# Optimization experiments

Hardware: AMD Instinct MI355X
Metric: run time of the kernel (lower is better)

The kernel has to match this reference:

```python
import jax, jax.numpy as jnp
import numpy as np

N_NODES, N_EDGES, N_GRAPHS = 20000, 640000, 16
D_NODE = D_EDGE = D_GLOBAL = 64
IN_DIM, LATENT, OUT_DIM = 256, 128, 64


def setup_inputs() -> dict:
    key = jax.random.key(0)
    ks = jax.random.split(key, 12)
    node_attr = jax.random.normal(ks[0], (N_NODES, D_NODE), dtype=jnp.float32)
    edge_attr = jax.random.normal(ks[1], (N_EDGES, D_EDGE), dtype=jnp.float32)
    global_attr = jax.random.normal(ks[2], (N_GRAPHS, D_GLOBAL), dtype=jnp.float32)
    node_mask = jax.random.uniform(ks[3], (N_NODES,), dtype=jnp.float32)
    edge_mask = jax.random.uniform(ks[4], (N_EDGES,), dtype=jnp.float32)
    edge_index = jax.random.randint(ks[5], (2, N_EDGES), 0, N_NODES, dtype=jnp.int64)
    eg_index = jax.random.randint(ks[6], (N_EDGES,), 0, N_GRAPHS, dtype=jnp.int64)
    # MLP params: Linear(IN_DIM, LATENT) -> ReLU -> Linear(LATENT, OUT_DIM)
    s1 = 1.0 / np.sqrt(IN_DIM)
    s2 = 1.0 / np.sqrt(LATENT)
    W1 = jax.random.uniform(ks[7], (IN_DIM, LATENT), minval=-s1, maxval=s1, dtype=jnp.float32)
    b1 = jax.random.uniform(ks[8], (LATENT,), minval=-s1, maxval=s1, dtype=jnp.float32)
    W2 = jax.random.uniform(ks[9], (LATENT, OUT_DIM), minval=-s2, maxval=s2, dtype=jnp.float32)
    b2 = jax.random.uniform(ks[10], (OUT_DIM,), minval=-s2, maxval=s2, dtype=jnp.float32)
    return {"node_attr": node_attr, "edge_attr": edge_attr, "global_attr": global_attr,
            "node_mask": node_mask, "edge_mask": edge_mask,
            "edge_index": edge_index, "eg_index": eg_index,
            "W1": W1, "b1": b1, "W2": W2, "b2": b2}


def reference(node_attr, edge_attr, global_attr, node_mask, edge_mask,
              edge_index, eg_index, W1, b1, W2, b2):
    senders, receivers = edge_index[0], edge_index[1]
    masked_nodes = node_attr * node_mask[:, None]          # [N, d_n]
    senders_attr = masked_nodes[senders]                   # [E, d_n] gather
    receivers_attr = masked_nodes[receivers]               # [E, d_n] gather
    globals_exp = global_attr[eg_index]                    # [E, d_g] gather
    collected = jnp.concatenate(
        [edge_attr, senders_attr, receivers_attr, globals_exp], axis=-1)  # [E, IN_DIM]
    h = jax.nn.relu(collected @ W1 + b1)                   # [E, LATENT]
    out = h @ W2 + b2                                      # [E, OUT_DIM]
    return edge_mask[:, None] * out
```

## Files before the change

kernel.cpp:

```cpp
#include <hip/hip_runtime.h>
#include <stdint.h>

typedef __attribute__((ext_vector_type(8))) short short8;
typedef __attribute__((ext_vector_type(4))) float floatx4;
typedef unsigned short ushort_t;

#define E_TOTAL 640000
#define M_BLK   128
#define XS_LD   264
#define HS_LD   136

__device__ __forceinline__ unsigned short f2h(float f){
    _Float16 h = (_Float16)f;
    union { _Float16 h; unsigned short u; } v; v.h = h; return v.u;
}
__device__ __forceinline__ unsigned pk2h(float a, float b){
    return (unsigned)f2h(a) | ((unsigned)f2h(b) << 16);
}

__global__ void repack_w(const float* __restrict__ W1,
                         const float* __restrict__ W2,
                         ushort_t* __restrict__ W1p,
                         ushort_t* __restrict__ W2p){
    int tid = blockIdx.x * 256 + threadIdx.x;
    if (tid < 8*8*64){
        int kt = tid >> 9, nt = (tid >> 6) & 7, l = tid & 63;
        int q = l >> 4, c = l & 15;
        ushort_t tmp[8];
        #pragma unroll
        for (int j = 0; j < 8; j++)
            tmp[j] = f2h(W1[(kt*32 + q*8 + j)*128 + nt*16 + c]);
        #pragma unroll
        for (int j = 0; j < 8; j++) W1p[tid*8 + j] = tmp[j];
    } else if (tid < 8*8*64 + 4*4*64){
        int t = tid - 8*8*64;
        int kt = t >> 8, nt = (t >> 6) & 3, l = t & 63;
        int q = l >> 4, c = l & 15;
        ushort_t tmp[8];
        #pragma unroll
        for (int j = 0; j < 8; j++)
            tmp[j] = f2h(W2[(kt*32 + q*8 + j)*64 + nt*16 + c]);
        #pragma unroll
        for (int j = 0; j < 8; j++) W2p[t*8 + j] = tmp[j];
    }
}

__global__ __launch_bounds__(512, 4)
void edge_mlp(const float* __restrict__ node_attr,
              const float* __restrict__ edge_attr,
              const float* __restrict__ global_attr,
              const float* __restrict__ node_mask,
              const float* __restrict__ edge_mask,
              const int*   __restrict__ edge_index,
              const int*   __restrict__ eg_index,
              const float* __restrict__ b1,
              const float* __restrict__ b2,
              const ushort_t* __restrict__ W1p,
              const ushort_t* __restrict__ W2p,
              float*       __restrict__ out){
    __shared__ ushort_t Xs[M_BLK * XS_LD];
    ushort_t* Hs = Xs;

    const int tid = threadIdx.x;
    const int e0  = blockIdx.x * M_BLK;

    {
        const float4* src = (const float4*)(edge_attr + (size_t)e0 * 64);
        #pragma unroll
        for (int k = 0; k < 4; k++){
            int idx = tid + k*512;
            int r = idx >> 4, c = idx & 15;
            float4 v = src[idx];
            uint2 o; o.x = pk2h(v.x, v.y); o.y = pk2h(v.z, v.w);
            *(uint2*)&Xs[r*XS_LD + c*4] = o;
        }
    }
    {
        #pragma unroll
        for (int k = 0; k < 4; k++){
            int idx = tid + k*512; int r = idx >> 4, c = idx & 15;
            int g = eg_index[e0 + r];
            const float4* src = (const float4*)(global_attr + (size_t)g * 64);
            float4 v = src[c];
            uint2 o; o.x = pk2h(v.x, v.y); o.y = pk2h(v.z, v.w);
            *(uint2*)&Xs[r*XS_LD + 192 + c*4] = o;
        }
    }
    {
        int r = tid >> 2, seg = (tid >> 1) & 1, half = tid & 1;
        int idx = edge_index[seg*E_TOTAL + e0 + r];
        float m = node_mask[idx];
        const float4* src = (const float4*)(node_attr + (size_t)idx * 64) + half*8;
        ushort_t* dst = &Xs[r*XS_LD + 64 + seg*64 + half*32];
        #pragma unroll
        for (int c2 = 0; c2 < 8; c2++){
            float4 v = src[c2];
            uint2 o; o.x = pk2h(v.x*m, v.y*m); o.y = pk2h(v.z*m, v.w*m);
            *(uint2*)(dst + c2*4) = o;
        }
    }
    __syncthreads();

    const int w  = tid >> 6, lane = tid & 63;
    const int q  = lane >> 4, cc = lane & 15;
    const int mt0 = (w >> 2) * 4;
    const int nt0 = (w & 3) * 2;

    floatx4 acc[4][2];
    #pragma unroll
    for (int i = 0; i < 4; i++)
        #pragma unroll
        for (int j = 0; j < 2; j++) acc[i][j] = (floatx4){0.f,0.f,0.f,0.f};

    const short8* W1v = (const short8*)W1p;
    #pragma unroll
    for (int kt = 0; kt < 8; kt++){
        short8 b[2];
        #pragma unroll
        for (int j = 0; j < 2; j++) b[j] = W1v[(kt*8 + nt0 + j)*64 + lane];
        #pragma unroll
        for (int i = 0; i < 4; i++){
            const short8 a = *(const short8*)&Xs[((mt0 + i)*16 + cc)*XS_LD + kt*32 + q*8];
            #pragma unroll
            for (int j = 0; j < 2; j++)
                acc[i][j] = __builtin_amdgcn_mfma_f32_16x16x32_f16(a, b[j], acc[i][j], 0, 0, 0);
        }
    }
    __syncthreads();

    #pragma unroll
    for (int j = 0; j < 2; j++){
        int col = (nt0 + j)*16 + cc;
        float bb = b1[col];
        #pragma unroll
        for (int i = 0; i < 4; i++){
            int rowb = (mt0 + i)*16 + q*4;
            #pragma unroll
            for (int r = 0; r < 4; r++){
                float v = acc[i][j][r] + bb;
                v = v > 0.f ? v : 0.f;
                Hs[(rowb + r)*HS_LD + col] = f2h(v);
            }
        }
    }
    __syncthreads();

    const int mt20 = (w >> 1) * 2;
    const int nt20 = (w & 1) * 2;

    floatx4 acc2[2][2];
    #pragma unroll
    for (int i = 0; i < 2; i++)
        #pragma unroll
        for (int j = 0; j < 2; j++) acc2[i][j] = (floatx4){0.f,0.f,0.f,0.f};

    const short8* W2v = (const short8*)W2p;
    #pragma unroll
    for (int kt = 0; kt < 4; kt++){
        short8 b[2];
        #pragma unroll
        for (int j = 0; j < 2; j++) b[j] = W2v[(kt*4 + nt20 + j)*64 + lane];
        #pragma unroll
        for (int i = 0; i < 2; i++){
            const short8 a = *(const short8*)&Hs[((mt20 + i)*16 + cc)*HS_LD + kt*32 + q*8];
            #pragma unroll
            for (int j = 0; j < 2; j++)
                acc2[i][j] = __builtin_amdgcn_mfma_f32_16x16x32_f16(a, b[j], acc2[i][j], 0, 0, 0);
        }
    }

    float bb2[2];
    #pragma unroll
    for (int j = 0; j < 2; j++) bb2[j] = b2[(nt20 + j)*16 + cc];
    #pragma unroll
    for (int i = 0; i < 2; i++){
        #pragma unroll
        for (int r = 0; r < 4; r++){
            int row = (mt20 + i)*16 + q*4 + r;
            float em = edge_mask[e0 + row];
            size_t base = (size_t)(e0 + row) * 64;
            #pragma unroll
            for (int j = 0; j < 2; j++){
                float v = (acc2[i][j][r] + bb2[j]) * em;
                out[base + (nt20 + j)*16 + cc] = v;
            }
        }
    }
}

extern "C" void kernel_launch(void* const* d_in, const int* in_sizes, int n_in,
                              void* d_out, int out_size, void* d_ws, size_t ws_size,
                              hipStream_t stream){
    const float* node_attr   = (const float*)d_in[0];
    const float* edge_attr   = (const float*)d_in[1];
    const float* global_attr = (const float*)d_in[2];
    const float* node_mask   = (const float*)d_in[3];
    const float* edge_mask   = (const float*)d_in[4];
    const int*   edge_index  = (const int*)d_in[5];
    const int*   eg_index    = (const int*)d_in[6];
    const float* W1          = (const float*)d_in[7];
    const float* b1          = (const float*)d_in[8];
    const float* W2          = (const float*)d_in[9];
    const float* b2          = (const float*)d_in[10];

    ushort_t* W1p = (ushort_t*)d_ws;
    ushort_t* W2p = W1p + 8*8*64*8;

    repack_w<<<20, 256, 0, stream>>>(W1, W2, W1p, W2p);
    edge_mlp<<<E_TOTAL / M_BLK, 512, 0, stream>>>(
        node_attr, edge_attr, global_attr, node_mask, edge_mask,
        edge_index, eg_index, b1, b2, W1p, W2p, (float*)d_out);
}
```

Baseline: 381.6 us.

## Make edge MLP kernel persistent with register-prefetched gathers for next tile

Switches from one block per 128-edge tile to a persistent grid of 512 blocks that loop over tiles. While the MFMA stages of the current tile run, the node, edge and global rows for the next tile are loaded into registers, and the indices are fetched two tiles ahead. This aims to hide global gather latency behind compute and to amortize bias loads and block launch cost. In exchange it raises register pressure with launch_bounds(512,4), which may cause spills or lower occupancy, and it relies on only 512 blocks to keep the device busy.

```diff
diff --git a/kernel.cpp b/kernel.cpp
--- a/kernel.cpp
+++ b/kernel.cpp
@@ -7,6 +7,8 @@
 
 #define E_TOTAL 640000
 #define M_BLK   128
+#define N_TILES (E_TOTAL / M_BLK)
+#define GRID_P  512
 #define XS_LD   264
 #define HS_LD   136
 
@@ -61,130 +63,203 @@
     __shared__ ushort_t Xs[M_BLK * XS_LD];
     ushort_t* Hs = Xs;
 
-    const int tid = threadIdx.x;
-    const int e0  = blockIdx.x * M_BLK;
+    const int tid  = threadIdx.x;
+    const int w    = tid >> 6, lane = tid & 63;
+    const int q    = lane >> 4, cc = lane & 15;
+    const int mt0  = (w >> 2) * 4;
+    const int nt0  = (w & 3) * 2;
+    const int mt20 = (w >> 1) * 2;
+    const int nt20 = (w & 1) * 2;
+
+    const int nr = tid >> 2, nseg = (tid >> 1) & 1, nhalf = tid & 1;
+
+    float bb1v[2], bb2v[2];
+    #pragma unroll
+    for (int j = 0; j < 2; j++){
+        bb1v[j] = b1[(nt0  + j)*16 + cc];
+        bb2v[j] = b2[(nt20 + j)*16 + cc];
+    }
+
+    const short8* W1v = (const short8*)W1p;
+    const short8* W2v = (const short8*)W2p;
+
+    int t = blockIdx.x;
+
+    uint2 pn16[8];
+    uint2 pe16[4];
+    uint2 pg16[4];
+    int   ei_n;
+    int   eg_n[4];
 
     {
-        const float4* src = (const float4*)(edge_attr + (size_t)e0 * 64);
+        size_t e0 = (size_t)t * M_BLK;
+        int ei = edge_index[nseg*E_TOTAL + e0 + nr];
+        int eg[4];
+        #pragma unroll
+        for (int k = 0; k < 4; k++) eg[k] = eg_index[e0 + ((tid + k*512) >> 4)];
+        float nm = node_mask[ei];
+        const floatx4* nsrc = (const floatx4*)(node_attr + (size_t)ei*64) + nhalf*8;
+        floatx4 nraw[8], eraw[4], graw[4];
+        #pragma unroll
+        for (int c2 = 0; c2 < 8; c2++) nraw[c2] = nsrc[c2];
+        const floatx4* esrc = (const floatx4*)(edge_attr + e0*64);
+        #pragma unroll
+        for (int k = 0; k < 4; k++) eraw[k] = esrc[tid + k*512];
+        #pragma unroll
+        for (int k = 0; k < 4; k++)
+            graw[k] = ((const floatx4*)(global_attr + (size_t)eg[k]*64))[(tid + k*512) & 15];
+        #pragma unroll
+        for (int c2 = 0; c2 < 8; c2++){
+            pn16[c2].x = pk2h(nraw[c2].x*nm, nraw[c2].y*nm);
+            pn16[c2].y = pk2h(nraw[c2].z*nm, nraw[c2].w*nm);
+        }
         #pragma unroll
         for (int k = 0; k < 4; k++){
-            int idx = tid + k*512;
-            int r = idx >> 4, c = idx & 15;
-            float4 v = src[idx];
-            uint2 o; o.x = pk2h(v.x, v.y); o.y = pk2h(v.z, v.w);
-            *(uint2*)&Xs[r*XS_LD + c*4] = o;
-        }
-    }
-    {
+            pe16[k].x = pk2h(eraw[k].x, eraw[k].y); pe16[k].y = pk2h(eraw[k].z, eraw[k].w);
+            pg16[k].x = pk2h(graw[k].x, graw[k].y); pg16[k].y = pk2h(graw[k].z, graw[k].w);
+        }
+    }
+    ei_n = 0; eg_n[0] = eg_n[1] = eg_n[2] = eg_n[3] = 0;
+    if (t + GRID_P < N_TILES){
+        size_t e0n = (size_t)(t + GRID_P) * M_BLK;
+        ei_n = edge_index[nseg*E_TOTAL + e0n + nr];
+        #pragma unroll
+        for (int k = 0; k < 4; k++) eg_n[k] = eg_index[e0n + ((tid + k*512) >> 4)];
+    }
+
+    for (; t < N_TILES; t += GRID_P){
+        const size_t e0 = (size_t)t * M_BLK;
+        const bool hn  = (t +   GRID_P < N_TILES);
+        const bool hn2 = (t + 2*GRID_P < N_TILES);
+
+        __syncthreads();
+
+        {
+            ushort_t* dst = &Xs[nr*XS_LD + 64 + nseg*64 + nhalf*32];
+            #pragma unroll
+            for (int c2 = 0; c2 < 8; c2++) *(uint2*)(dst + c2*4) = pn16[c2];
+        }
         #pragma unroll
         for (int k = 0; k < 4; k++){
             int idx = tid + k*512; int r = idx >> 4, c = idx & 15;
-            int g = eg_index[e0 + r];
-            const float4* src = (const float4*)(global_attr + (size_t)g * 64);
-            float4 v = src[c];
-            uint2 o; o.x = pk2h(v.x, v.y); o.y = pk2h(v.z, v.w);
-            *(uint2*)&Xs[r*XS_LD + 192 + c*4] = o;
-        }
-    }
-    {
-        int r = tid >> 2, seg = (tid >> 1) & 1, half = tid & 1;
-        int idx = edge_index[seg*E_TOTAL + e0 + r];
-        float m = node_mask[idx];
-        const float4* src = (const float4*)(node_attr + (size_t)idx * 64) + half*8;
-        ushort_t* dst = &Xs[r*XS_LD + 64 + seg*64 + half*32];
-        #pragma unroll
-        for (int c2 = 0; c2 < 8; c2++){
-            float4 v = src[c2];
-            uint2 o; o.x = pk2h(v.x*m, v.y*m); o.y = pk2h(v.z*m, v.w*m);
-            *(uint2*)(dst + c2*4) = o;
-        }
-    }
-    __syncthreads();
-
-    const int w  = tid >> 6, lane = tid & 63;
-    const int q  = lane >> 4, cc = lane & 15;
-    const int mt0 = (w >> 2) * 4;
-    const int nt0 = (w & 3) * 2;
-
-    floatx4 acc[4][2];
-    #pragma unroll
-    for (int i = 0; i < 4; i++)
-        #pragma unroll
-        for (int j = 0; j < 2; j++) acc[i][j] = (floatx4){0.f,0.f,0.f,0.f};
-
-    const short8* W1v = (const short8*)W1p;
-    #pragma unroll
-    for (int kt = 0; kt < 8; kt++){
-        short8 b[2];
-        #pragma unroll
-        for (int j = 0; j < 2; j++) b[j] = W1v[(kt*8 + nt0 + j)*64 + lane];
-        #pragma unroll
-        for (int i = 0; i < 4; i++){
-            const short8 a = *(const short8*)&Xs[((mt0 + i)*16 + cc)*XS_LD + kt*32 + q*8];
-            #pragma unroll
-            for (int j = 0; j < 2; j++)
-                acc[i][j] = __builtin_amdgcn_mfma_f32_16x16x32_f16(a, b[j], acc[i][j], 0, 0, 0);
-        }
-    }
-    __syncthreads();
-
-    #pragma unroll
-    for (int j = 0; j < 2; j++){
-        int col = (nt0 + j)*16 + cc;
-        float bb = b1[col];
-        #pragma unroll
-        for (int i = 0; i < 4; i++){
-            int rowb = (mt0 + i)*16 + q*4;
+            *(uint2*)&Xs[r*XS_LD + c*4]       = pe16[k];
+            *(uint2*)&Xs[r*XS_LD + 192 + c*4] = pg16[k];
+        }
+        __syncthreads();
+
+        float nm_n = 0.f;
+        floatx4 nraw[8];
+        if (hn){
+            nm_n = node_mask[ei_n];
+            const floatx4* nsrc = (const floatx4*)(node_attr + (size_t)ei_n*64) + nhalf*8;
+            #pragma unroll
+            for (int c2 = 0; c2 < 8; c2++) nraw[c2] = nsrc[c2];
+        }
+        int ei_n2 = 0, eg_n2[4] = {0,0,0,0};
+        if (hn2){
+            size_t e0n2 = (size_t)(t + 2*GRID_P) * M_BLK;
+            ei_n2 = edge_index[nseg*E_TOTAL + e0n2 + nr];
+            #pragma unroll
+            for (int k = 0; k < 4; k++) eg_n2[k] = eg_index[e0n2 + ((tid + k*512) >> 4)];
+        }
+
+        floatx4 acc[4][2];
+        #pragma unroll
+        for (int i = 0; i < 4; i++)
+            #pragma unroll
+            for (int j = 0; j < 2; j++) acc[i][j] = (floatx4){0.f,0.f,0.f,0.f};
+
+        #pragma unroll
+        for (int kt = 0; kt < 8; kt++){
+            short8 b[2];
+            #pragma unroll
+            for (int j = 0; j < 2; j++) b[j] = W1v[(kt*8 + nt0 + j)*64 + lane];
+            #pragma unroll
+            for (int i = 0; i < 4; i++){
+                const short8 a = *(const short8*)&Xs[((mt0 + i)*16 + cc)*XS_LD + kt*32 + q*8];
+                #pragma unroll
+                for (int j = 0; j < 2; j++)
+                    acc[i][j] = __builtin_amdgcn_mfma_f32_16x16x32_f16(a, b[j], acc[i][j], 0, 0, 0);
+            }
+        }
+
+        floatx4 eraw[4], graw[4];
+        if (hn){
+            #pragma unroll
+            for (int c2 = 0; c2 < 8; c2++){
+                pn16[c2].x = pk2h(nraw[c2].x*nm_n, nraw[c2].y*nm_n);
+                pn16[c2].y = pk2h(nraw[c2].z*nm_n, nraw[c2].w*nm_n);
+            }
+            size_t e0n = (size_t)(t + GRID_P) * M_BLK;
+            const floatx4* esrc = (const floatx4*)(edge_attr + e0n*64);
+            #pragma unroll
+            for (int k = 0; k < 4; k++) eraw[k] = esrc[tid + k*512];
+            #pragma unroll
+            for (int k = 0; k < 4; k++)
+                graw[k] = ((const floatx4*)(global_attr + (size_t)eg_n[k]*64))[(tid + k*512) & 15];
+        }
+
+        __syncthreads();
+
+        #pragma unroll
+        for (int j = 0; j < 2; j++){
+            int col = (nt0 + j)*16 + cc;
+            #pragma unroll
+            for (int i = 0; i < 4; i++){
+                int rowb = (mt0 + i)*16 + q*4;
+                #pragma unroll
+                for (int r = 0; r < 4; r++){
+                    float v = acc[i][j][r] + bb1v[j];
+                    v = v > 0.f ? v : 0.f;
+                    Hs[(rowb + r)*HS_LD + col] = f2h(v);
+                }
+            }
+        }
+        __syncthreads();
+
+        floatx4 acc2[2][2];
+        #pragma unroll
+        for (int i = 0; i < 2; i++)
+            #pragma unroll
+            for (int j = 0; j < 2; j++) acc2[i][j] = (floatx4){0.f,0.f,0.f,0.f};
+
+        #pragma unroll
+        for (int kt = 0; kt < 4; kt++){
+            short8 b[2];
+            #pragma unroll
+            for (int j = 0; j < 2; j++) b[j] = W2v[(kt*4 + nt20 + j)*64 + lane];
+            #pragma unroll
+            for (int i = 0; i < 2; i++){
+                const short8 a = *(const short8*)&Hs[((mt20 + i)*16 + cc)*HS_LD + kt*32 + q*8];
+                #pragma unroll
+                for (int j = 0; j < 2; j++)
+                    acc2[i][j] = __builtin_amdgcn_mfma_f32_16x16x32_f16(a, b[j], acc2[i][j], 0, 0, 0);
+            }
+        }
+
+        #pragma unroll
+        for (int i = 0; i < 2; i++){
             #pragma unroll
             for (int r = 0; r < 4; r++){
-                float v = acc[i][j][r] + bb;
-                v = v > 0.f ? v : 0.f;
-                Hs[(rowb + r)*HS_LD + col] = f2h(v);
-            }
-        }
-    }
-    __syncthreads();
-
-    const int mt20 = (w >> 1) * 2;
-    const int nt20 = (w & 1) * 2;
-
-    floatx4 acc2[2][2];
-    #pragma unroll
-    for (int i = 0; i < 2; i++)
-        #pragma unroll
-        for (int j = 0; j < 2; j++) acc2[i][j] = (floatx4){0.f,0.f,0.f,0.f};
-
-    const short8* W2v = (const short8*)W2p;
-    #pragma unroll
-    for (int kt = 0; kt < 4; kt++){
-        short8 b[2];
-        #pragma unroll
-        for (int j = 0; j < 2; j++) b[j] = W2v[(kt*4 + nt20 + j)*64 + lane];
-        #pragma unroll
-        for (int i = 0; i < 2; i++){
-            const short8 a = *(const short8*)&Hs[((mt20 + i)*16 + cc)*HS_LD + kt*32 + q*8];
-            #pragma unroll
-            for (int j = 0; j < 2; j++)
-                acc2[i][j] = __builtin_amdgcn_mfma_f32_16x16x32_f16(a, b[j], acc2[i][j], 0, 0, 0);
-        }
-    }
-
-    float bb2[2];
-    #pragma unroll
-    for (int j = 0; j < 2; j++) bb2[j] = b2[(nt20 + j)*16 + cc];
-    #pragma unroll
-    for (int i = 0; i < 2; i++){
-        #pragma unroll
-        for (int r = 0; r < 4; r++){
-            int row = (mt20 + i)*16 + q*4 + r;
-            float em = edge_mask[e0 + row];
-            size_t base = (size_t)(e0 + row) * 64;
-            #pragma unroll
-            for (int j = 0; j < 2; j++){
-                float v = (acc2[i][j][r] + bb2[j]) * em;
-                out[base + (nt20 + j)*16 + cc] = v;
-            }
-        }
+                int row = (mt20 + i)*16 + q*4 + r;
+                float em = edge_mask[e0 + row];
+                size_t base = (size_t)(e0 + row) * 64;
+                #pragma unroll
+                for (int j = 0; j < 2; j++)
+                    out[base + (nt20 + j)*16 + cc] = (acc2[i][j][r] + bb2v[j]) * em;
+            }
+        }
+
+        if (hn){
+            #pragma unroll
+            for (int k = 0; k < 4; k++){
+                pe16[k].x = pk2h(eraw[k].x, eraw[k].y); pe16[k].y = pk2h(eraw[k].z, eraw[k].w);
+                pg16[k].x = pk2h(graw[k].x, graw[k].y); pg16[k].y = pk2h(graw[k].z, graw[k].w);
+            }
+        }
+        ei_n = ei_n2;
+        #pragma unroll
+        for (int k = 0; k < 4; k++) eg_n[k] = eg_n2[k];
     }
 }
 
@@ -207,7 +282,7 @@
     ushort_t* W2p = W1p + 8*8*64*8;
 
     repack_w<<<20, 256, 0, stream>>>(W1, W2, W1p, W2p);
-    edge_mlp<<<E_TOTAL / M_BLK, 512, 0, stream>>>(
+    edge_mlp<<<GRID_P, 512, 0, stream>>>(
         node_attr, edge_attr, global_attr, node_mask, edge_mask,
         edge_index, eg_index, b1, b2, W1p, W2p, (float*)d_out);
 }
```

Result: slower. 840.3 us (+120.2%).

## Pre-convert masked node and global tables to fp16 and preload W1 fragments

Applied to the files above, without the earlier changes.

Adds a prep kernel that applies the node mask and converts node and global attribute tables to fp16 once. The main kernel then gathers half-width rows without per-edge mask multiplies or conversions. It also hoists all W1 B-fragments into registers before the gather phase so their loads overlap. The cost is an extra launch and workspace table, plus higher register pressure from holding 16 short8 fragments, which could reduce occupancy. A fallback path keeps the old kernel when the workspace is too small.

```diff
diff --git a/kernel.cpp b/kernel.cpp
--- a/kernel.cpp
+++ b/kernel.cpp
@@ -6,7 +6,9 @@
 typedef unsigned short ushort_t;
 
 #define E_TOTAL 640000
+#define N_NODES 20000
 #define M_BLK   128
+#define N_TILES (E_TOTAL / M_BLK)
 #define XS_LD   264
 #define HS_LD   136
 
@@ -45,11 +47,35 @@
     }
 }
 
+__global__ void prep_tables(const float* __restrict__ node_attr,
+                            const float* __restrict__ node_mask,
+                            const float* __restrict__ global_attr,
+                            ushort_t* __restrict__ node16,
+                            ushort_t* __restrict__ glob16){
+    int gid = blockIdx.x * 256 + threadIdx.x;
+    if (gid < N_NODES * 8){
+        int r = gid >> 3, c8 = gid & 7;
+        float m = node_mask[r];
+        const float4* src = (const float4*)(node_attr + (size_t)r*64 + c8*8);
+        float4 a = src[0], b = src[1];
+        uint4 o;
+        o.x = pk2h(a.x*m, a.y*m); o.y = pk2h(a.z*m, a.w*m);
+        o.z = pk2h(b.x*m, b.y*m); o.w = pk2h(b.z*m, b.w*m);
+        *(uint4*)(node16 + (size_t)r*64 + c8*8) = o;
+    } else if (gid < N_NODES * 8 + 16 * 8){
+        int t = gid - N_NODES * 8;
+        int r = t >> 3, c8 = t & 7;
+        const float4* src = (const float4*)(global_attr + (size_t)r*64 + c8*8);
+        float4 a = src[0], b = src[1];
+        uint4 o;
+        o.x = pk2h(a.x, a.y); o.y = pk2h(a.z, a.w);
+        o.z = pk2h(b.x, b.y); o.w = pk2h(b.z, b.w);
+        *(uint4*)(glob16 + (size_t)r*64 + c8*8) = o;
+    }
+}
+
 __global__ __launch_bounds__(512, 4)
-void edge_mlp(const float* __restrict__ node_attr,
-              const float* __restrict__ edge_attr,
-              const float* __restrict__ global_attr,
-              const float* __restrict__ node_mask,
+void edge_mlp(const float* __restrict__ edge_attr,
               const float* __restrict__ edge_mask,
               const int*   __restrict__ edge_index,
               const int*   __restrict__ eg_index,
@@ -57,13 +83,152 @@
               const float* __restrict__ b2,
               const ushort_t* __restrict__ W1p,
               const ushort_t* __restrict__ W2p,
+              const ushort_t* __restrict__ node16,
+              const ushort_t* __restrict__ glob16,
               float*       __restrict__ out){
     __shared__ ushort_t Xs[M_BLK * XS_LD];
     ushort_t* Hs = Xs;
 
     const int tid = threadIdx.x;
     const int e0  = blockIdx.x * M_BLK;
-
+    const int w   = tid >> 6, lane = tid & 63;
+    const int q   = lane >> 4, cc = lane & 15;
+    const int mt0 = (w >> 2) * 4;
+    const int nt0 = (w & 3) * 2;
+
+    const short8* W1v = (const short8*)W1p;
+    short8 wb[8][2];
+    #pragma unroll
+    for (int kt = 0; kt < 8; kt++)
+        #pragma unroll
+        for (int j = 0; j < 2; j++)
+            wb[kt][j] = W1v[(kt*8 + nt0 + j)*64 + lane];
+
+    {
+        const float4* src = (const float4*)(edge_attr + (size_t)e0 * 64);
+        #pragma unroll
+        for (int k = 0; k < 4; k++){
+            int idx = tid + k*512;
+            int r = idx >> 4, c = idx & 15;
+            float4 v = src[idx];
+            uint2 o; o.x = pk2h(v.x, v.y); o.y = pk2h(v.z, v.w);
+            *(uint2*)&Xs[r*XS_LD + c*4] = o;
+        }
+    }
+    {
+        #pragma unroll
+        for (int k = 0; k < 2; k++){
+            int idx = tid + k*512;
+            int r = idx >> 3, c = idx & 7;
+            int g = eg_index[e0 + r];
+            uint4 v = *(const uint4*)(glob16 + (size_t)g*64 + c*8);
+            *(uint4*)&Xs[r*XS_LD + 192 + c*8] = v;
+        }
+    }
+    {
+        int r = tid >> 2, seg = (tid >> 1) & 1, half = tid & 1;
+        int idx = edge_index[seg*E_TOTAL + e0 + r];
+        const uint4* nsrc = (const uint4*)(node16 + (size_t)idx*64 + half*32);
+        ushort_t* dst = &Xs[r*XS_LD + 64 + seg*64 + half*32];
+        #pragma unroll
+        for (int c2 = 0; c2 < 4; c2++)
+            *(uint4*)(dst + c2*8) = nsrc[c2];
+    }
+    __syncthreads();
+
+    floatx4 acc[4][2];
+    #pragma unroll
+    for (int i = 0; i < 4; i++)
+        #pragma unroll
+        for (int j = 0; j < 2; j++) acc[i][j] = (floatx4){0.f,0.f,0.f,0.f};
+
+    #pragma unroll
+    for (int kt = 0; kt < 8; kt++){
+        #pragma unroll
+        for (int i = 0; i < 4; i++){
+            const short8 a = *(const short8*)&Xs[((mt0 + i)*16 + cc)*XS_LD + kt*32 + q*8];
+            #pragma unroll
+            for (int j = 0; j < 2; j++)
+                acc[i][j] = __builtin_amdgcn_mfma_f32_16x16x32_f16(a, wb[kt][j], acc[i][j], 0, 0, 0);
+        }
+    }
+    __syncthreads();
+
+    #pragma unroll
+    for (int j = 0; j < 2; j++){
+        int col = (nt0 + j)*16 + cc;
+        float bb = b1[col];
+        #pragma unroll
+        for (int i = 0; i < 4; i++){
+            int rowb = (mt0 + i)*16 + q*4;
+            #pragma unroll
+            for (int r = 0; r < 4; r++){
+                float v = acc[i][j][r] + bb;
+                v = v > 0.f ? v : 0.f;
+                Hs[(rowb + r)*HS_LD + col] = f2h(v);
+            }
+        }
+    }
+    __syncthreads();
+
+    const int mt20 = (w >> 1) * 2;
+    const int nt20 = (w & 1) * 2;
+
+    floatx4 acc2[2][2];
+    #pragma unroll
+    for (int i = 0; i < 2; i++)
+        #pragma unroll
+        for (int j = 0; j < 2; j++) acc2[i][j] = (floatx4){0.f,0.f,0.f,0.f};
+
+    const short8* W2v = (const short8*)W2p;
+    #pragma unroll
+    for (int kt = 0; kt < 4; kt++){
+        short8 b[2];
+        #pragma unroll
+        for (int j = 0; j < 2; j++) b[j] = W2v[(kt*4 + nt20 + j)*64 + lane];
+        #pragma unroll
+        for (int i = 0; i < 2; i++){
+            const short8 a = *(const short8*)&Hs[((mt20 + i)*16 + cc)*HS_LD + kt*32 + q*8];
+            #pragma unroll
+            for (int j = 0; j < 2; j++)
+                acc2[i][j] = __builtin_amdgcn_mfma_f32_16x16x32_f16(a, b[j], acc2[i][j], 0, 0, 0);
+        }
+    }
+
+    float bb2[2];
+    #pragma unroll
+    for (int j = 0; j < 2; j++) bb2[j] = b2[(nt20 + j)*16 + cc];
+    #pragma unroll
+    for (int i = 0; i < 2; i++){
+        #pragma unroll
+        for (int r = 0; r < 4; r++){
+            int row = (mt20 + i)*16 + q*4 + r;
+            float em = edge_mask[e0 + row];
+            size_t base = (size_t)(e0 + row) * 64;
+            #pragma unroll
+            for (int j = 0; j < 2; j++)
+                out[base + (nt20 + j)*16 + cc] = (acc2[i][j][r] + bb2[j]) * em;
+        }
+    }
+}
+
+__global__ __launch_bounds__(512, 4)
+void edge_mlp_fb(const float* __restrict__ node_attr,
+                 const float* __restrict__ edge_attr,
+                 const float* __restrict__ global_attr,
+                 const float* __restrict__ node_mask,
+                 const float* __restrict__ edge_mask,
+                 const int*   __restrict__ edge_index,
+                 const int*   __restrict__ eg_index,
+                 const float* __restrict__ b1,
+                 const float* __restrict__ b2,
+                 const ushort_t* __restrict__ W1p,
+                 const ushort_t* __restrict__ W2p,
+                 float*       __restrict__ out){
+    __shared__ ushort_t Xs[M_BLK * XS_LD];
+    ushort_t* Hs = Xs;
+    const int tid = threadIdx.x;
+    const int e0  = blockIdx.x * M_BLK;
     {
         const float4* src = (const float4*)(edge_attr + (size_t)e0 * 64);
         #pragma unroll
@@ -180,10 +345,8 @@
             float em = edge_mask[e0 + row];
             size_t base = (size_t)(e0 + row) * 64;
             #pragma unroll
-            for (int j = 0; j < 2; j++){
-                float v = (acc2[i][j][r] + bb2[j]) * em;
-                out[base + (nt20 + j)*16 + cc] = v;
-            }
+            for (int j = 0; j < 2; j++)
+                out[base + (nt20 + j)*16 + cc] = (acc2[i][j][r] + bb2[j]) * em;
         }
     }
 }
@@ -205,9 +368,21 @@
 
     ushort_t* W1p = (ushort_t*)d_ws;
     ushort_t* W2p = W1p + 8*8*64*8;
+    ushort_t* node16 = W2p + 4*4*64*8;
+    ushort_t* glob16 = node16 + (size_t)N_NODES*64;
+
+    size_t need = (size_t)(8*8*64*8 + 4*4*64*8 + N_NODES*64 + 16*64) * sizeof(ushort_t);
 
     repack_w<<<20, 256, 0, stream>>>(W1, W2, W1p, W2p);
-    edge_mlp<<<E_TOTAL / M_BLK, 512, 0, stream>>>(
-        node_attr, edge_attr, global_attr, node_mask, edge_mask,
-        edge_index, eg_index, b1, b2, W1p, W2p, (float*)d_out);
-}
+    if (ws_size >= need){
+        prep_tables<<<(N_NODES*8 + 16*8 + 255)/256, 256, 0, stream>>>(
+            node_attr, node_mask, global_attr, node16, glob16);
+        edge_mlp<<<N_TILES, 512, 0, stream>>>(
+            edge_attr, edge_mask, edge_index, eg_index,
+            b1, b2, W1p, W2p, node16, glob16, (float*)d_out);
+    } else {
+        edge_mlp_fb<<<N_TILES, 512, 0, stream>>>(
+            node_attr, edge_attr, global_attr, node_mask, edge_mask,
+            edge_index, eg_index, b1, b2, W1p, W2p, (float*)d_out);
+    }
+}
```

Measured after the change: 337.0 us. 11.7% less time.
